# Optimization experiments

Hardware: AMD Instinct MI355X
Metric: run time of the kernel (lower is better)

Reference implementation:

```python
import jax, jax.numpy as jnp
import numpy as np

S, B, E, DH, OUT = 1024, 128, 1024, 1024, 1024

def setup_inputs() -> dict:
    key = jax.random.key(0)
    k1, k2, k3, k4, k5, k6 = jax.random.split(key, 6)
    sc1 = 1.0 / np.sqrt(DH)
    sc2 = 1.0 / np.sqrt(E + DH)
    return {
        "ingr_outputs": jax.random.normal(k1, (S, B, E), dtype=jnp.float32),
        "decoder_hidden": jax.random.normal(k2, (1, B, DH), dtype=jnp.float32),
        "W_proj": jax.random.uniform(k3, (E, DH), jnp.float32, -sc1, sc1),
        "b_proj": jax.random.uniform(k4, (E,), jnp.float32, -sc1, sc1),
        "W_out": jax.random.uniform(k5, (OUT, E + DH), jnp.float32, -sc2, sc2),
        "b_out": jax.random.uniform(k6, (OUT,), jnp.float32, -sc2, sc2),
    }

def reference(ingr_outputs, decoder_hidden, W_proj, b_proj, W_out, b_out):
    # ingr_outputs: [S, B, E]; decoder_hidden: [T, B, DH] (T = 1)
    ref = decoder_hidden
    dh = jnp.einsum('tbd,ed->tbe', decoder_hidden, W_proj) + b_proj  # [T,B,E]
    scores = jnp.einsum('sbe,tbe->bts', ingr_outputs, dh)            # [B,T,S]
    attn = jax.nn.softmax(scores, axis=2)
    context = jnp.einsum('bts,sbe->tbe', attn, ingr_outputs)         # [T,B,E]
    concat = jnp.concatenate([context, ref], axis=2)                 # [T,B,E+DH]
    out = jnp.einsum('tbc,oc->tbo', concat, W_out) + b_out           # [T,B,OUT]
    return out
```

## Files before the change

### kernel.cpp

```cpp
#include <hip/hip_runtime.h>
#include <math.h>

#define SS 1024
#define BB 128
#define EE 1024
#define DHH 1024
#define OO 1024
#define NCHUNK 8
#define ROWS_PER_CHUNK (SS / NCHUNK)
#define NWAVES 4
#define ROWS_PER_WAVE (ROWS_PER_CHUNK / NWAVES)

__device__ __forceinline__ float wave_reduce_sum(float v) {
    v += __shfl_xor(v, 32);
    v += __shfl_xor(v, 16);
    v += __shfl_xor(v, 8);
    v += __shfl_xor(v, 4);
    v += __shfl_xor(v, 2);
    v += __shfl_xor(v, 1);
    return v;
}

__global__ __launch_bounds__(256) void init_bias_kernel(float* __restrict__ dst,
                                                        const float* __restrict__ bias,
                                                        int total) {
    int i = blockIdx.x * 256 + threadIdx.x;
    if (i < total) dst[i] = bias[i & 1023];
}

__global__ __launch_bounds__(256) void gemm_nt_splitk(const float* __restrict__ A,
                                                      const float* __restrict__ B,
                                                      float* __restrict__ C,
                                                      int M, int N, int K, int Kc) {
    __shared__ float As[32][33];
    __shared__ float Bs[32][33];
    const int n0 = blockIdx.x * 32;
    const int m0 = blockIdx.y * 32;
    const int k0 = blockIdx.z * Kc;
    const int tid = threadIdx.x;
    const int lr = tid >> 3;
    const int lc = (tid & 7) << 2;
    const int tm = (tid >> 4) << 1;
    const int tn = (tid & 15) << 1;
    float acc00 = 0.f, acc01 = 0.f, acc10 = 0.f, acc11 = 0.f;
    for (int kk = k0; kk < k0 + Kc; kk += 32) {
        float4 av = *(const float4*)(A + (size_t)(m0 + lr) * K + kk + lc);
        float4 bv = *(const float4*)(B + (size_t)(n0 + lr) * K + kk + lc);
        As[lr][lc] = av.x; As[lr][lc + 1] = av.y; As[lr][lc + 2] = av.z; As[lr][lc + 3] = av.w;
        Bs[lr][lc] = bv.x; Bs[lr][lc + 1] = bv.y; Bs[lr][lc + 2] = bv.z; Bs[lr][lc + 3] = bv.w;
        __syncthreads();
#pragma unroll
        for (int j = 0; j < 32; ++j) {
            float a0 = As[tm][j], a1 = As[tm + 1][j];
            float b0 = Bs[tn][j], b1 = Bs[tn + 1][j];
            acc00 = fmaf(a0, b0, acc00);
            acc01 = fmaf(a0, b1, acc01);
            acc10 = fmaf(a1, b0, acc10);
            acc11 = fmaf(a1, b1, acc11);
        }
        __syncthreads();
    }
    float* c0 = C + (size_t)(m0 + tm) * N + n0 + tn;
    unsafeAtomicAdd(c0, acc00);
    unsafeAtomicAdd(c0 + 1, acc01);
    unsafeAtomicAdd(c0 + N, acc10);
    unsafeAtomicAdd(c0 + N + 1, acc11);
}

__global__ __launch_bounds__(256) void flash_attn_kernel(
        const float* __restrict__ ingr,
        const float* __restrict__ dh,
        float* __restrict__ pctx,
        float* __restrict__ pml)
{
    const int chunk = blockIdx.x;
    const int b = blockIdx.y;
    const int tid = threadIdx.x;
    const int wave = tid >> 6;
    const int lane = tid & 63;

    const float* dhb = dh + (size_t)b * EE + (lane << 2);
    const float4 d0 = *(const float4*)(dhb);
    const float4 d1 = *(const float4*)(dhb + 256);
    const float4 d2 = *(const float4*)(dhb + 512);
    const float4 d3 = *(const float4*)(dhb + 768);

    float m = -INFINITY, l = 0.f;
    float4 c0 = make_float4(0.f, 0.f, 0.f, 0.f);
    float4 c1 = make_float4(0.f, 0.f, 0.f, 0.f);
    float4 c2 = make_float4(0.f, 0.f, 0.f, 0.f);
    float4 c3 = make_float4(0.f, 0.f, 0.f, 0.f);

    const int s0 = chunk * ROWS_PER_CHUNK + wave * ROWS_PER_WAVE;
    const size_t row_stride = (size_t)BB * EE;
    const float* rp = ingr + ((size_t)s0 * BB + b) * EE + (lane << 2);

    float4 x0 = *(const float4*)(rp);
    float4 x1 = *(const float4*)(rp + 256);
    float4 x2 = *(const float4*)(rp + 512);
    float4 x3 = *(const float4*)(rp + 768);

    for (int j = 0; j < ROWS_PER_WAVE; ++j) {
        const float* np = rp + ((j < ROWS_PER_WAVE - 1) ? row_stride : 0);
        float4 y0 = *(const float4*)(np);
        float4 y1 = *(const float4*)(np + 256);
        float4 y2 = *(const float4*)(np + 512);
        float4 y3 = *(const float4*)(np + 768);

        float p0 = x0.x * d0.x + x0.y * d0.y + x0.z * d0.z + x0.w * d0.w;
        float p1 = x1.x * d1.x + x1.y * d1.y + x1.z * d1.z + x1.w * d1.w;
        float p2 = x2.x * d2.x + x2.y * d2.y + x2.z * d2.z + x2.w * d2.w;
        float p3 = x3.x * d3.x + x3.y * d3.y + x3.z * d3.z + x3.w * d3.w;
        float p = (p0 + p1) + (p2 + p3);
        p = wave_reduce_sum(p);

        float mn = fmaxf(m, p);
        float alpha = __expf(m - mn);
        float pe = __expf(p - mn);
        l = l * alpha + pe;
        c0.x = fmaf(pe, x0.x, c0.x * alpha);
        c0.y = fmaf(pe, x0.y, c0.y * alpha);
        c0.z = fmaf(pe, x0.z, c0.z * alpha);
        c0.w = fmaf(pe, x0.w, c0.w * alpha);
        c1.x = fmaf(pe, x1.x, c1.x * alpha);
        c1.y = fmaf(pe, x1.y, c1.y * alpha);
        c1.z = fmaf(pe, x1.z, c1.z * alpha);
        c1.w = fmaf(pe, x1.w, c1.w * alpha);
        c2.x = fmaf(pe, x2.x, c2.x * alpha);
        c2.y = fmaf(pe, x2.y, c2.y * alpha);
        c2.z = fmaf(pe, x2.z, c2.z * alpha);
        c2.w = fmaf(pe, x2.w, c2.w * alpha);
        c3.x = fmaf(pe, x3.x, c3.x * alpha);
        c3.y = fmaf(pe, x3.y, c3.y * alpha);
        c3.z = fmaf(pe, x3.z, c3.z * alpha);
        c3.w = fmaf(pe, x3.w, c3.w * alpha);
        m = mn;

        x0 = y0; x1 = y1; x2 = y2; x3 = y3;
        rp = np;
    }

    __shared__ float cbuf[NWAVES][EE];
    __shared__ float smm[NWAVES], sll[NWAVES];
    float4* cw = (float4*)&cbuf[wave][0];
    cw[lane] = c0;
    cw[64 + lane] = c1;
    cw[128 + lane] = c2;
    cw[192 + lane] = c3;
    if (lane == 0) { smm[wave] = m; sll[wave] = l; }
    __syncthreads();

    const float M = fmaxf(fmaxf(smm[0], smm[1]), fmaxf(smm[2], smm[3]));
    const float w0 = __expf(smm[0] - M);
    const float w1 = __expf(smm[1] - M);
    const float w2 = __expf(smm[2] - M);
    const float w3 = __expf(smm[3] - M);
    const float L = sll[0] * w0 + sll[1] * w1 + sll[2] * w2 + sll[3] * w3;

    float4 a0 = ((const float4*)&cbuf[0][0])[tid];
    float4 a1 = ((const float4*)&cbuf[1][0])[tid];
    float4 a2 = ((const float4*)&cbuf[2][0])[tid];
    float4 a3 = ((const float4*)&cbuf[3][0])[tid];
    float4 r;
    r.x = a0.x * w0 + a1.x * w1 + a2.x * w2 + a3.x * w3;
    r.y = a0.y * w0 + a1.y * w1 + a2.y * w2 + a3.y * w3;
    r.z = a0.z * w0 + a1.z * w1 + a2.z * w2 + a3.z * w3;
    r.w = a0.w * w0 + a1.w * w1 + a2.w * w2 + a3.w * w3;

    float4* dst = (float4*)(pctx + ((size_t)b * NCHUNK + chunk) * EE);
    dst[tid] = r;
    if (tid == 0) {
        pml[((size_t)b * NCHUNK + chunk) * 2] = M;
        pml[((size_t)b * NCHUNK + chunk) * 2 + 1] = L;
    }
}

__global__ __launch_bounds__(256) void combine_kernel(
        const float* __restrict__ pctx,
        const float* __restrict__ pml,
        const float* __restrict__ dec,
        float* __restrict__ concat)
{
    const int b = blockIdx.x;
    const int tid = threadIdx.x;
    float M = -INFINITY;
#pragma unroll
    for (int c = 0; c < NCHUNK; ++c)
        M = fmaxf(M, pml[((size_t)b * NCHUNK + c) * 2]);
    float w[NCHUNK];
    float L = 0.f;
#pragma unroll
    for (int c = 0; c < NCHUNK; ++c) {
        w[c] = __expf(pml[((size_t)b * NCHUNK + c) * 2] - M);
        L += pml[((size_t)b * NCHUNK + c) * 2 + 1] * w[c];
    }
    const float invL = 1.f / L;
    float4 r = make_float4(0.f, 0.f, 0.f, 0.f);
#pragma unroll
    for (int c = 0; c < NCHUNK; ++c) {
        float4 v = ((const float4*)(pctx + ((size_t)b * NCHUNK + c) * EE))[tid];
        r.x = fmaf(v.x, w[c], r.x);
        r.y = fmaf(v.y, w[c], r.y);
        r.z = fmaf(v.z, w[c], r.z);
        r.w = fmaf(v.w, w[c], r.w);
    }
    r.x *= invL; r.y *= invL; r.z *= invL; r.w *= invL;
    float* crow = concat + (size_t)b * (EE + DHH);
    ((float4*)crow)[tid] = r;
    float4 dv = ((const float4*)(dec + (size_t)b * DHH))[tid];
    ((float4*)(crow + EE))[tid] = dv;
}

extern "C" void kernel_launch(void* const* d_in, const int* in_sizes, int n_in,
                              void* d_out, int out_size, void* d_ws, size_t ws_size,
                              hipStream_t stream) {
    const float* ingr = (const float*)d_in[0];
    const float* dec  = (const float*)d_in[1];
    const float* Wp   = (const float*)d_in[2];
    const float* bp   = (const float*)d_in[3];
    const float* Wo   = (const float*)d_in[4];
    const float* bo   = (const float*)d_in[5];
    float* out = (float*)d_out;

    float* dhbuf  = (float*)d_ws;
    float* pctx   = dhbuf + (size_t)BB * EE;
    float* pml    = pctx + (size_t)BB * NCHUNK * EE;
    float* concat = pml + (size_t)BB * NCHUNK * 2;

    init_bias_kernel<<<(BB * EE) / 256, 256, 0, stream>>>(dhbuf, bp, BB * EE);
    gemm_nt_splitk<<<dim3(EE / 32, BB / 32, 4), 256, 0, stream>>>(
        dec, Wp, dhbuf, BB, EE, DHH, DHH / 4);

    flash_attn_kernel<<<dim3(NCHUNK, BB), 256, 0, stream>>>(ingr, dhbuf, pctx, pml);

    combine_kernel<<<BB, 256, 0, stream>>>(pctx, pml, dec, concat);

    init_bias_kernel<<<(BB * OO) / 256, 256, 0, stream>>>(out, bo, BB * OO);
    gemm_nt_splitk<<<dim3(OO / 32, BB / 32, 4), 256, 0, stream>>>(
        concat, Wo, out, BB, OO, EE + DHH, (EE + DHH) / 4);
}
```

Baseline: 744.2 us.

## Retile split-K GEMMs with partial buffers and unroll attention rows by two

Replaces the 32x32 atomic split-K GEMM with a 64x64 tile, 4x4 per-thread register-blocked GEMM that uses 16 K-splits, register prefetch of the next K slab and a transposed shared layout for float4 reads. Partial sums go to workspace and a separate reduce kernel adds the bias, replacing atomics and the bias-init kernels. The flash attention loop now handles two sequence rows per iteration, interleaving their shuffle reductions and sharing one rescale. This adds workspace traffic for the partials and more registers per thread.

```diff
diff --git a/kernel.cpp b/kernel.cpp
--- a/kernel.cpp
+++ b/kernel.cpp
@@ -10,61 +10,86 @@
 #define ROWS_PER_CHUNK (SS / NCHUNK)
 #define NWAVES 4
 #define ROWS_PER_WAVE (ROWS_PER_CHUNK / NWAVES)
-
-__device__ __forceinline__ float wave_reduce_sum(float v) {
-    v += __shfl_xor(v, 32);
-    v += __shfl_xor(v, 16);
-    v += __shfl_xor(v, 8);
-    v += __shfl_xor(v, 4);
-    v += __shfl_xor(v, 2);
-    v += __shfl_xor(v, 1);
-    return v;
-}
-
-__global__ __launch_bounds__(256) void init_bias_kernel(float* __restrict__ dst,
-                                                        const float* __restrict__ bias,
-                                                        int total) {
-    int i = blockIdx.x * 256 + threadIdx.x;
-    if (i < total) dst[i] = bias[i & 1023];
-}
-
-__global__ __launch_bounds__(256) void gemm_nt_splitk(const float* __restrict__ A,
-                                                      const float* __restrict__ B,
-                                                      float* __restrict__ C,
-                                                      int M, int N, int K, int Kc) {
-    __shared__ float As[32][33];
-    __shared__ float Bs[32][33];
-    const int n0 = blockIdx.x * 32;
-    const int m0 = blockIdx.y * 32;
-    const int k0 = blockIdx.z * Kc;
+#define ZSPLIT 16
+
+__global__ __launch_bounds__(256) void gemm_nt_partk(const float* __restrict__ A,
+                                                     const float* __restrict__ B,
+                                                     float* __restrict__ part,
+                                                     int M, int N, int K, int Kc) {
+    __shared__ float As[32][68];
+    __shared__ float Bs[32][68];
+    const int n0 = blockIdx.x * 64;
+    const int m0 = blockIdx.y * 64;
+    const int z  = blockIdx.z;
+    const int k0 = z * Kc;
     const int tid = threadIdx.x;
-    const int lr = tid >> 3;
-    const int lc = (tid & 7) << 2;
-    const int tm = (tid >> 4) << 1;
-    const int tn = (tid & 15) << 1;
-    float acc00 = 0.f, acc01 = 0.f, acc10 = 0.f, acc11 = 0.f;
-    for (int kk = k0; kk < k0 + Kc; kk += 32) {
-        float4 av = *(const float4*)(A + (size_t)(m0 + lr) * K + kk + lc);
-        float4 bv = *(const float4*)(B + (size_t)(n0 + lr) * K + kk + lc);
-        As[lr][lc] = av.x; As[lr][lc + 1] = av.y; As[lr][lc + 2] = av.z; As[lr][lc + 3] = av.w;
-        Bs[lr][lc] = bv.x; Bs[lr][lc + 1] = bv.y; Bs[lr][lc + 2] = bv.z; Bs[lr][lc + 3] = bv.w;
+    const int r  = tid & 63;
+    const int kc = (tid >> 6) << 2;
+    const int tm = ((tid >> 4) & 15) << 2;
+    const int tn = (tid & 15) << 2;
+
+    const float* Ap = A + (size_t)(m0 + r) * K + k0;
+    const float* Bp = B + (size_t)(n0 + r) * K + k0;
+
+    float4 a0 = *(const float4*)(Ap + kc);
+    float4 a1 = *(const float4*)(Ap + 16 + kc);
+    float4 b0 = *(const float4*)(Bp + kc);
+    float4 b1 = *(const float4*)(Bp + 16 + kc);
+
+    float acc[4][4] = {};
+    const int nkt = Kc >> 5;
+    for (int kt = 0; kt < nkt; ++kt) {
         __syncthreads();
-#pragma unroll
-        for (int j = 0; j < 32; ++j) {
-            float a0 = As[tm][j], a1 = As[tm + 1][j];
-            float b0 = Bs[tn][j], b1 = Bs[tn + 1][j];
-            acc00 = fmaf(a0, b0, acc00);
-            acc01 = fmaf(a0, b1, acc01);
-            acc10 = fmaf(a1, b0, acc10);
-            acc11 = fmaf(a1, b1, acc11);
+        As[kc + 0][r] = a0.x; As[kc + 1][r] = a0.y; As[kc + 2][r] = a0.z; As[kc + 3][r] = a0.w;
+        As[kc + 16][r] = a1.x; As[kc + 17][r] = a1.y; As[kc + 18][r] = a1.z; As[kc + 19][r] = a1.w;
+        Bs[kc + 0][r] = b0.x; Bs[kc + 1][r] = b0.y; Bs[kc + 2][r] = b0.z; Bs[kc + 3][r] = b0.w;
+        Bs[kc + 16][r] = b1.x; Bs[kc + 17][r] = b1.y; Bs[kc + 18][r] = b1.z; Bs[kc + 19][r] = b1.w;
+
+        float4 na0 = make_float4(0.f, 0.f, 0.f, 0.f), na1 = na0, nb0 = na0, nb1 = na0;
+        if (kt + 1 < nkt) {
+            const float* Ap2 = Ap + ((kt + 1) << 5);
+            const float* Bp2 = Bp + ((kt + 1) << 5);
+            na0 = *(const float4*)(Ap2 + kc);
+            na1 = *(const float4*)(Ap2 + 16 + kc);
+            nb0 = *(const float4*)(Bp2 + kc);
+            nb1 = *(const float4*)(Bp2 + 16 + kc);
         }
         __syncthreads();
-    }
-    float* c0 = C + (size_t)(m0 + tm) * N + n0 + tn;
-    unsafeAtomicAdd(c0, acc00);
-    unsafeAtomicAdd(c0 + 1, acc01);
-    unsafeAtomicAdd(c0 + N, acc10);
-    unsafeAtomicAdd(c0 + N + 1, acc11);
+#pragma unroll
+        for (int j = 0; j < 32; ++j) {
+            const float4 av = *(const float4*)&As[j][tm];
+            const float4 bv = *(const float4*)&Bs[j][tn];
+            const float a_[4] = {av.x, av.y, av.z, av.w};
+            const float b_[4] = {bv.x, bv.y, bv.z, bv.w};
+#pragma unroll
+            for (int i = 0; i < 4; ++i)
+#pragma unroll
+                for (int jj = 0; jj < 4; ++jj)
+                    acc[i][jj] = fmaf(a_[i], b_[jj], acc[i][jj]);
+        }
+        a0 = na0; a1 = na1; b0 = nb0; b1 = nb1;
+    }
+
+    float* P = part + ((size_t)z * M + m0 + tm) * N + n0 + tn;
+#pragma unroll
+    for (int i = 0; i < 4; ++i) {
+        float4 v = make_float4(acc[i][0], acc[i][1], acc[i][2], acc[i][3]);
+        *(float4*)(P + (size_t)i * N) = v;
+    }
+}
+
+__global__ __launch_bounds__(256) void reduce_splitk(const float* __restrict__ part,
+                                                     const float* __restrict__ bias,
+                                                     float* __restrict__ dst,
+                                                     int MN4, int Z) {
+    const int i = blockIdx.x * 256 + threadIdx.x;
+    if (i >= MN4) return;
+    float4 s = ((const float4*)bias)[i & 255];
+    for (int zz = 0; zz < Z; ++zz) {
+        float4 v = ((const float4*)part)[(size_t)zz * MN4 + i];
+        s.x += v.x; s.y += v.y; s.z += v.z; s.w += v.w;
+    }
+    ((float4*)dst)[i] = s;
 }
 
 __global__ __launch_bounds__(256) void flash_attn_kernel(
@@ -87,56 +112,75 @@
 
     float m = -INFINITY, l = 0.f;
     float4 c0 = make_float4(0.f, 0.f, 0.f, 0.f);
-    float4 c1 = make_float4(0.f, 0.f, 0.f, 0.f);
-    float4 c2 = make_float4(0.f, 0.f, 0.f, 0.f);
-    float4 c3 = make_float4(0.f, 0.f, 0.f, 0.f);
+    float4 c1 = c0, c2 = c0, c3 = c0;
 
     const int s0 = chunk * ROWS_PER_CHUNK + wave * ROWS_PER_WAVE;
-    const size_t row_stride = (size_t)BB * EE;
+    const size_t rs = (size_t)BB * EE;
     const float* rp = ingr + ((size_t)s0 * BB + b) * EE + (lane << 2);
 
-    float4 x0 = *(const float4*)(rp);
-    float4 x1 = *(const float4*)(rp + 256);
-    float4 x2 = *(const float4*)(rp + 512);
-    float4 x3 = *(const float4*)(rp + 768);
-
-    for (int j = 0; j < ROWS_PER_WAVE; ++j) {
-        const float* np = rp + ((j < ROWS_PER_WAVE - 1) ? row_stride : 0);
-        float4 y0 = *(const float4*)(np);
-        float4 y1 = *(const float4*)(np + 256);
-        float4 y2 = *(const float4*)(np + 512);
-        float4 y3 = *(const float4*)(np + 768);
-
-        float p0 = x0.x * d0.x + x0.y * d0.y + x0.z * d0.z + x0.w * d0.w;
-        float p1 = x1.x * d1.x + x1.y * d1.y + x1.z * d1.z + x1.w * d1.w;
-        float p2 = x2.x * d2.x + x2.y * d2.y + x2.z * d2.z + x2.w * d2.w;
-        float p3 = x3.x * d3.x + x3.y * d3.y + x3.z * d3.z + x3.w * d3.w;
-        float p = (p0 + p1) + (p2 + p3);
-        p = wave_reduce_sum(p);
-
-        float mn = fmaxf(m, p);
-        float alpha = __expf(m - mn);
-        float pe = __expf(p - mn);
-        l = l * alpha + pe;
-        c0.x = fmaf(pe, x0.x, c0.x * alpha);
-        c0.y = fmaf(pe, x0.y, c0.y * alpha);
-        c0.z = fmaf(pe, x0.z, c0.z * alpha);
-        c0.w = fmaf(pe, x0.w, c0.w * alpha);
-        c1.x = fmaf(pe, x1.x, c1.x * alpha);
-        c1.y = fmaf(pe, x1.y, c1.y * alpha);
-        c1.z = fmaf(pe, x1.z, c1.z * alpha);
-        c1.w = fmaf(pe, x1.w, c1.w * alpha);
-        c2.x = fmaf(pe, x2.x, c2.x * alpha);
-        c2.y = fmaf(pe, x2.y, c2.y * alpha);
-        c2.z = fmaf(pe, x2.z, c2.z * alpha);
-        c2.w = fmaf(pe, x2.w, c2.w * alpha);
-        c3.x = fmaf(pe, x3.x, c3.x * alpha);
-        c3.y = fmaf(pe, x3.y, c3.y * alpha);
-        c3.z = fmaf(pe, x3.z, c3.z * alpha);
-        c3.w = fmaf(pe, x3.w, c3.w * alpha);
+    float4 xa0 = *(const float4*)(rp);
+    float4 xa1 = *(const float4*)(rp + 256);
+    float4 xa2 = *(const float4*)(rp + 512);
+    float4 xa3 = *(const float4*)(rp + 768);
+    float4 xb0 = *(const float4*)(rp + rs);
+    float4 xb1 = *(const float4*)(rp + rs + 256);
+    float4 xb2 = *(const float4*)(rp + rs + 512);
+    float4 xb3 = *(const float4*)(rp + rs + 768);
+
+    const int NB = ROWS_PER_WAVE / 2;
+    for (int jb = 0; jb < NB; ++jb) {
+        const float* np = (jb < NB - 1) ? rp + 2 * rs : rp;
+        float4 ya0 = *(const float4*)(np);
+        float4 ya1 = *(const float4*)(np + 256);
+        float4 ya2 = *(const float4*)(np + 512);
+        float4 ya3 = *(const float4*)(np + 768);
+        float4 yb0 = *(const float4*)(np + rs);
+        float4 yb1 = *(const float4*)(np + rs + 256);
+        float4 yb2 = *(const float4*)(np + rs + 512);
+        float4 yb3 = *(const float4*)(np + rs + 768);
+
+        float pa = fmaf(xa0.x, d0.x, fmaf(xa0.y, d0.y, fmaf(xa0.z, d0.z, xa0.w * d0.w)));
+        pa = fmaf(xa1.x, d1.x, fmaf(xa1.y, d1.y, fmaf(xa1.z, d1.z, fmaf(xa1.w, d1.w, pa))));
+        float pa2 = fmaf(xa2.x, d2.x, fmaf(xa2.y, d2.y, fmaf(xa2.z, d2.z, xa2.w * d2.w)));
+        pa2 = fmaf(xa3.x, d3.x, fmaf(xa3.y, d3.y, fmaf(xa3.z, d3.z, fmaf(xa3.w, d3.w, pa2))));
+        pa += pa2;
+        float pb = fmaf(xb0.x, d0.x, fmaf(xb0.y, d0.y, fmaf(xb0.z, d0.z, xb0.w * d0.w)));
+        pb = fmaf(xb1.x, d1.x, fmaf(xb1.y, d1.y, fmaf(xb1.z, d1.z, fmaf(xb1.w, d1.w, pb))));
+        float pb2 = fmaf(xb2.x, d2.x, fmaf(xb2.y, d2.y, fmaf(xb2.z, d2.z, xb2.w * d2.w)));
+        pb2 = fmaf(xb3.x, d3.x, fmaf(xb3.y, d3.y, fmaf(xb3.z, d3.z, fmaf(xb3.w, d3.w, pb2))));
+        pb += pb2;
+
+#pragma unroll
+        for (int off = 32; off; off >>= 1) {
+            pa += __shfl_xor(pa, off);
+            pb += __shfl_xor(pb, off);
+        }
+
+        const float mn = fmaxf(m, fmaxf(pa, pb));
+        const float al = __expf(m - mn);
+        const float ea = __expf(pa - mn);
+        const float eb = __expf(pb - mn);
+        l = fmaf(l, al, ea + eb);
+        c0.x = fmaf(eb, xb0.x, fmaf(ea, xa0.x, c0.x * al));
+        c0.y = fmaf(eb, xb0.y, fmaf(ea, xa0.y, c0.y * al));
+        c0.z = fmaf(eb, xb0.z, fmaf(ea, xa0.z, c0.z * al));
+        c0.w = fmaf(eb, xb0.w, fmaf(ea, xa0.w, c0.w * al));
+        c1.x = fmaf(eb, xb1.x, fmaf(ea, xa1.x, c1.x * al));
+        c1.y = fmaf(eb, xb1.y, fmaf(ea, xa1.y, c1.y * al));
+        c1.z = fmaf(eb, xb1.z, fmaf(ea, xa1.z, c1.z * al));
+        c1.w = fmaf(eb, xb1.w, fmaf(ea, xa1.w, c1.w * al));
+        c2.x = fmaf(eb, xb2.x, fmaf(ea, xa2.x, c2.x * al));
+        c2.y = fmaf(eb, xb2.y, fmaf(ea, xa2.y, c2.y * al));
+        c2.z = fmaf(eb, xb2.z, fmaf(ea, xa2.z, c2.z * al));
+        c2.w = fmaf(eb, xb2.w, fmaf(ea, xa2.w, c2.w * al));
+        c3.x = fmaf(eb, xb3.x, fmaf(ea, xa3.x, c3.x * al));
+        c3.y = fmaf(eb, xb3.y, fmaf(ea, xa3.y, c3.y * al));
+        c3.z = fmaf(eb, xb3.z, fmaf(ea, xa3.z, c3.z * al));
+        c3.w = fmaf(eb, xb3.w, fmaf(ea, xa3.w, c3.w * al));
         m = mn;
 
-        x0 = y0; x1 = y1; x2 = y2; x3 = y3;
+        xa0 = ya0; xa1 = ya1; xa2 = ya2; xa3 = ya3;
+        xb0 = yb0; xb1 = yb1; xb2 = yb2; xb3 = yb3;
         rp = np;
     }
 
@@ -226,16 +270,20 @@
     float* pctx   = dhbuf + (size_t)BB * EE;
     float* pml    = pctx + (size_t)BB * NCHUNK * EE;
     float* concat = pml + (size_t)BB * NCHUNK * 2;
-
-    init_bias_kernel<<<(BB * EE) / 256, 256, 0, stream>>>(dhbuf, bp, BB * EE);
-    gemm_nt_splitk<<<dim3(EE / 32, BB / 32, 4), 256, 0, stream>>>(
-        dec, Wp, dhbuf, BB, EE, DHH, DHH / 4);
+    float* part1  = concat + (size_t)BB * (EE + DHH);
+    float* part2  = part1 + (size_t)ZSPLIT * BB * EE;
+
+    const int MN4 = BB * EE / 4;
+
+    gemm_nt_partk<<<dim3(EE / 64, BB / 64, ZSPLIT), 256, 0, stream>>>(
+        dec, Wp, part1, BB, EE, DHH, DHH / ZSPLIT);
+    reduce_splitk<<<MN4 / 256, 256, 0, stream>>>(part1, bp, dhbuf, MN4, ZSPLIT);
 
     flash_attn_kernel<<<dim3(NCHUNK, BB), 256, 0, stream>>>(ingr, dhbuf, pctx, pml);
 
     combine_kernel<<<BB, 256, 0, stream>>>(pctx, pml, dec, concat);
 
-    init_bias_kernel<<<(BB * OO) / 256, 256, 0, stream>>>(out, bo, BB * OO);
-    gemm_nt_splitk<<<dim3(OO / 32, BB / 32, 4), 256, 0, stream>>>(
-        concat, Wo, out, BB, OO, EE + DHH, (EE + DHH) / 4);
-}
+    gemm_nt_partk<<<dim3(OO / 64, BB / 64, ZSPLIT), 256, 0, stream>>>(
+        concat, Wo, part2, BB, OO, EE + DHH, (EE + DHH) / ZSPLIT);
+    reduce_splitk<<<MN4 / 256, 256, 0, stream>>>(part2, bo, out, MN4, ZSPLIT);
+}
```

Measured after the change: 719.1 us. 3.4% less time.
